# Optimization experiments

Hardware: AMD Instinct MI355X
Metric: run time of the kernel (lower is better)

The kernel has to match this reference:

```python
import jax, jax.numpy as jnp
import numpy as np

R, D, H, NLAYERS = 128, 64, 64, 3
B, N = 64, 1024
INIT_W = 0.1


def setup_inputs() -> dict:
    key = jax.random.key(0)
    ks = jax.random.split(key, 10)
    x = jax.random.normal(ks[0], (B, D, N), dtype=jnp.float32)
    L = jax.random.randint(ks[1], (B, 1, N), 0, 2, dtype=jnp.int32)
    wq0 = INIT_W * jax.random.normal(ks[2], (R, D), dtype=jnp.float32)
    wqr = INIT_W * jax.random.normal(ks[3], (NLAYERS - 1, R, R), dtype=jnp.float32)
    wk0 = INIT_W * jax.random.normal(ks[4], (R, D), dtype=jnp.float32)
    wkr = INIT_W * jax.random.normal(ks[5], (NLAYERS - 1, R, R), dtype=jnp.float32)
    wv0 = INIT_W * jax.random.normal(ks[6], (R, D), dtype=jnp.float32)
    wvr = INIT_W * jax.random.normal(ks[7], (NLAYERS - 1, R, R), dtype=jnp.float32)
    wor = INIT_W * jax.random.normal(ks[8], (NLAYERS - 1, R, R), dtype=jnp.float32)
    wo_last = INIT_W * jax.random.normal(ks[9], (H, R), dtype=jnp.float32)
    return {"x": x, "L": L, "wq0": wq0, "wqr": wqr, "wk0": wk0, "wkr": wkr,
            "wv0": wv0, "wvr": wvr, "wor": wor, "wo_last": wo_last}


def reference(x, L, wq0, wqr, wk0, wkr, wv0, wvr, wor, wo_last):
    # x: [B, d, N]; L: [B, 1, N] neighbor mask (first row used)
    Lrow = L[:, 0, :].astype(jnp.float32)                      # [B, N]
    num_neighbors = jnp.sum((Lrow >= 1).astype(jnp.float32), axis=1)[:, None, None] + 1.0  # [B,1,1]
    scale = jnp.sqrt(num_neighbors)
    mask = Lrow[:, None, :]                                    # [B, 1, N], broadcast over r

    inp = x
    for layer in range(NLAYERS):
        Wq = wq0 if layer == 0 else wqr[layer - 1]
        Wk = wk0 if layer == 0 else wkr[layer - 1]
        Wv = wv0 if layer == 0 else wvr[layer - 1]
        # sigmoid-gated projections: [B, r, N]
        Q = jax.nn.sigmoid(jnp.einsum('rd,bdn->brn', Wq, inp))
        K = jax.nn.sigmoid(jnp.einsum('rd,bdn->brn', Wk, inp))
        V = jax.nn.sigmoid(jnp.einsum('rd,bdn->brn', Wv, inp))
        # degree-scaled softmax attention over agents: scores [B, N, N]
        A = jax.nn.softmax(jnp.einsum('brn,brm->bnm', Q, K) / scale, axis=-1)
        # o[b,r,n] = sum_m A[b,n,m] * V[b,r,m]  -> [B, r, N]
        o = jnp.einsum('bnm,brm->brn', A, V)
        Wo = wor[layer] if layer < NLAYERS - 1 else wo_last
        inp = jax.nn.silu(jnp.einsum('or,brn->bon', Wo, o))
        if layer != NLAYERS - 1:  # remask_bias=True
            inp = mask * inp
    return inp  # [B, h, N]
```

## Files before the change

kernel.cpp:

```cpp
#include <hip/hip_runtime.h>


typedef __bf16 bf16;
typedef bf16 bf16x2 __attribute__((ext_vector_type(2)));
typedef bf16 bf16x4 __attribute__((ext_vector_type(4)));
typedef bf16 bf16x8 __attribute__((ext_vector_type(8)));
typedef float f32x4 __attribute__((ext_vector_type(4)));
typedef float f32x16 __attribute__((ext_vector_type(16)));

#define MFMA32(a, b, c) __builtin_amdgcn_mfma_f32_32x32x16_bf16(a, b, c, 0, 0, 0)
#define ZERO16 {0,0,0,0,0,0,0,0,0,0,0,0,0,0,0,0}
#define LOG2E 1.44269504f

__device__ __forceinline__ float fast_exp2(float x) {
  return __builtin_amdgcn_exp2f(x);
}
__device__ __forceinline__ float fast_sigmoid(float x) {
  return __builtin_amdgcn_rcpf(1.0f + fast_exp2(-LOG2E * x));
}

__global__ __launch_bounds__(256) void prep_kernel(
    const int* __restrict__ L,
    const float* __restrict__ wq0, const float* __restrict__ wqr,
    const float* __restrict__ wk0, const float* __restrict__ wkr,
    const float* __restrict__ wv0, const float* __restrict__ wvr,
    const float* __restrict__ wor, const float* __restrict__ wo_last,
    float* __restrict__ scale_inv, float* __restrict__ biasv,
    bf16* __restrict__ wbf) {
  __shared__ int red[256];
  const int blk = blockIdx.x;
  const int tid = threadIdx.x;
  if (blk < 64) {
    int cnt = 0;
    for (int n = tid; n < 1024; n += 256) cnt += (L[blk * 1024 + n] >= 1) ? 1 : 0;
    red[tid] = cnt;
    __syncthreads();
    for (int s = 128; s > 0; s >>= 1) {
      if (tid < s) red[tid] += red[tid + s];
      __syncthreads();
    }
    if (tid == 0) {
      float iv = rsqrtf((float)red[0] + 1.0f);
      scale_inv[blk] = iv;
      biasv[blk] = fmaxf(0.0f, 128.0f * iv * LOG2E - 80.0f);
    }
  } else {
    for (int i = (blk - 64) * 256 + tid; i < 163840; i += 64 * 256) {
      float v;
      if      (i <   8192) v = wq0[i];
      else if (i <  40960) v = wqr[i - 8192];
      else if (i <  49152) v = wk0[i - 40960];
      else if (i <  81920) v = wkr[i - 49152];
      else if (i <  90112) v = wv0[i - 81920];
      else if (i < 122880) v = wvr[i - 90112];
      else if (i < 155648) v = wor[i - 122880];
      else                 v = wo_last[i - 155648];
      wbf[i] = (bf16)v;
    }
  }
}

__global__ __launch_bounds__(256) void xk0_kernel(
    const float* __restrict__ x, const bf16* __restrict__ Wk,
    const bf16* __restrict__ Wv, bf16* __restrict__ xT,
    bf16* __restrict__ Kt, bf16* __restrict__ Vn) {
  __shared__ float tile[64][65];
  __shared__ __attribute__((aligned(16))) bf16 inp_lds[64 * 72];
  const int tid = threadIdx.x;
  const int lane = tid & 63, wv = tid >> 6;
  const int la = lane & 31, hi = lane >> 5;
  const int b = blockIdx.x >> 4;
  const int t0 = (blockIdx.x & 15) * 64;

  {
    const int nl = tid & 63, dbase = (tid >> 6) * 16;
#pragma unroll
    for (int i = 0; i < 16; i++) {
      int d = dbase + i;
      tile[d][nl] = x[(size_t)(b * 64 + d) * 1024 + t0 + nl];
    }
  }
  __syncthreads();
  {
    const int dl = (tid & 31) * 2, nb = (tid >> 5) * 8;
#pragma unroll
    for (int i = 0; i < 8; i++) {
      int n = nb + i;
      bf16x2 pr = {(bf16)tile[dl][n], (bf16)tile[dl + 1][n]};
      *(bf16x2*)(xT + (size_t)(b * 1024 + t0 + n) * 64 + dl) = pr;
      *(bf16x2*)&inp_lds[n * 72 + dl] = pr;
    }
  }
  __syncthreads();

  const int sub = wv & 1;
  if (wv < 2) {
#pragma unroll
    for (int rt2 = 0; rt2 < 2; rt2++) {
      const int rt = 2 * sub + rt2;
      bf16x8 wf[4];
#pragma unroll
      for (int ks = 0; ks < 4; ks++)
        wf[ks] = *(const bf16x8*)(Wk + (size_t)(la + 32 * rt) * 64 + hi * 8 + ks * 16);
#pragma unroll
      for (int tt = 0; tt < 2; tt++) {
        f32x16 acc = ZERO16;
#pragma unroll
        for (int ks = 0; ks < 4; ks++) {
          bf16x8 bfr = *(const bf16x8*)&inp_lds[(la + 32 * tt) * 72 + hi * 8 + ks * 16];
          acc = MFMA32(wf[ks], bfr, acc);
        }
#pragma unroll
        for (int g = 0; g < 4; g++) {
          bf16x4 pk;
#pragma unroll
          for (int i = 0; i < 4; i++) pk[i] = (bf16)fast_sigmoid(acc[4 * g + i]);
          *(bf16x4*)(Kt + (size_t)(b * 1024 + t0 + 32 * tt + la) * 128 +
                     32 * rt + 8 * g + 4 * hi) = pk;
        }
      }
    }
  } else {
#pragma unroll
    for (int rc2 = 0; rc2 < 2; rc2++) {
      const int rc = 2 * sub + rc2;
      bf16x8 wf[4];
#pragma unroll
      for (int ks = 0; ks < 4; ks++)
        wf[ks] = *(const bf16x8*)(Wv + (size_t)(la + 32 * rc) * 64 + hi * 8 + ks * 16);
#pragma unroll
      for (int tt = 0; tt < 2; tt++) {
        f32x16 acc = ZERO16;
#pragma unroll
        for (int ks = 0; ks < 4; ks++) {
          bf16x8 afr = *(const bf16x8*)&inp_lds[(la + 32 * tt) * 72 + hi * 8 + ks * 16];
          acc = MFMA32(afr, wf[ks], acc);
        }
#pragma unroll
        for (int g = 0; g < 4; g++) {
          bf16x4 pk;
#pragma unroll
          for (int i = 0; i < 4; i++) pk[i] = (bf16)fast_sigmoid(acc[4 * g + i]);
          *(bf16x4*)(Vn + (size_t)(b * 128 + la + 32 * rc) * 1024 +
                     t0 + 32 * tt + 8 * g + 4 * hi) = pk;
        }
      }
    }
  }
}

template <int DIN>
__global__ __launch_bounds__(256) void kv_kernel(
    const bf16* __restrict__ inpT, const bf16* __restrict__ Wk,
    const bf16* __restrict__ Wv, bf16* __restrict__ Kt,
    bf16* __restrict__ Vn) {
  constexpr int SIN = DIN + 8;
  constexpr int KS = DIN / 16;
  constexpr int CPR = DIN / 8;
  __shared__ __attribute__((aligned(16))) bf16 inp_lds[64 * SIN];
  const int tid = threadIdx.x;
  const int lane = tid & 63, wv = tid >> 6;
  const int la = lane & 31, hi = lane >> 5;
  const int b = blockIdx.x >> 4;
  const int t0 = (blockIdx.x & 15) * 64;

  for (int i = tid; i < 64 * CPR; i += 256) {
    int row = i / CPR, c = i % CPR;
    *(bf16x8*)&inp_lds[row * SIN + c * 8] =
        *(const bf16x8*)(inpT + (size_t)(b * 1024 + t0 + row) * DIN + c * 8);
  }
  __syncthreads();

  const int sub = wv & 1;
  if (wv < 2) {
#pragma unroll
    for (int rt2 = 0; rt2 < 2; rt2++) {
      const int rt = 2 * sub + rt2;
      bf16x8 wf[KS];
#pragma unroll
      for (int ks = 0; ks < KS; ks++)
        wf[ks] = *(const bf16x8*)(Wk + (size_t)(la + 32 * rt) * DIN + hi * 8 + ks * 16);
#pragma unroll
      for (int tt = 0; tt < 2; tt++) {
        f32x16 acc = ZERO16;
#pragma unroll
        for (int ks = 0; ks < KS; ks++) {
          bf16x8 bfr = *(const bf16x8*)&inp_lds[(la + 32 * tt) * SIN + hi * 8 + ks * 16];
          acc = MFMA32(wf[ks], bfr, acc);
        }
#pragma unroll
        for (int g = 0; g < 4; g++) {
          bf16x4 pk;
#pragma unroll
          for (int i = 0; i < 4; i++) pk[i] = (bf16)fast_sigmoid(acc[4 * g + i]);
          *(bf16x4*)(Kt + (size_t)(b * 1024 + t0 + 32 * tt + la) * 128 +
                     32 * rt + 8 * g + 4 * hi) = pk;
        }
      }
    }
  } else {
#pragma unroll
    for (int rc2 = 0; rc2 < 2; rc2++) {
      const int rc = 2 * sub + rc2;
      bf16x8 wf[KS];
#pragma unroll
      for (int ks = 0; ks < KS; ks++)
        wf[ks] = *(const bf16x8*)(Wv + (size_t)(la + 32 * rc) * DIN + hi * 8 + ks * 16);
#pragma unroll
      for (int tt = 0; tt < 2; tt++) {
        f32x16 acc = ZERO16;
#pragma unroll
        for (int ks = 0; ks < KS; ks++) {
          bf16x8 afr = *(const bf16x8*)&inp_lds[(la + 32 * tt) * SIN + hi * 8 + ks * 16];
          acc = MFMA32(afr, wf[ks], acc);
        }
#pragma unroll
        for (int g = 0; g < 4; g++) {
          bf16x4 pk;
#pragma unroll
          for (int i = 0; i < 4; i++) pk[i] = (bf16)fast_sigmoid(acc[4 * g + i]);
          *(bf16x4*)(Vn + (size_t)(b * 128 + la + 32 * rc) * 1024 +
                     t0 + 32 * tt + 8 * g + 4 * hi) = pk;
        }
      }
    }
  }
}

template <int DIN>
__global__ __launch_bounds__(256, 2) void flash_kernel(
    const bf16* __restrict__ inpT, const bf16* __restrict__ Wq,
    const bf16* __restrict__ Kt, const bf16* __restrict__ Vn,
    const float* __restrict__ scale_inv, const float* __restrict__ biasv,
    const int* __restrict__ L, const bf16* __restrict__ Wo,
    void* __restrict__ outp, int last,
    const bf16* __restrict__ Wkn, const bf16* __restrict__ Wvn,
    bf16* __restrict__ Ktn, bf16* __restrict__ Vnn, int kvgen) {
  __shared__ __attribute__((aligned(16))) char smem[70656];
  bf16* K_lds = (bf16*)smem;
  bf16* V_lds = (bf16*)(smem + 17408);
  bf16* P_lds = (bf16*)(smem + 35840);

  const int tid = threadIdx.x;
  const int lane = tid & 63, wv = tid >> 6;
  const int la = lane & 31, hi = lane >> 5;
  const int xcd = blockIdx.x & 7;
  const int kk = blockIdx.x >> 3;
  const int b = xcd * 8 + (kk & 7);
  const int q0 = (kk >> 3) * 128;

  const float inv2 = scale_inv[b] * LOG2E;
  const float bb = biasv[b];

  {
    constexpr int SIN = DIN + 8;
    constexpr int KSD = DIN / 16;
    constexpr int CPR = DIN / 8;
    bf16* inp_s = (bf16*)smem;
    for (int i = tid; i < 128 * CPR; i += 256) {
      int row = i / CPR, c = i % CPR;
      *(bf16x8*)&inp_s[row * SIN + c * 8] =
          *(const bf16x8*)(inpT + (size_t)(b * 1024 + q0 + row) * DIN + c * 8);
    }
    __syncthreads();
    bf16* Q_lds = (bf16*)(smem + 35840);
    bf16x8 wf[KSD];
#pragma unroll
    for (int ks = 0; ks < KSD; ks++)
      wf[ks] = *(const bf16x8*)(Wq + (size_t)(la + 32 * wv) * DIN + hi * 8 + ks * 16);
#pragma unroll
    for (int nt = 0; nt < 4; nt++) {
      f32x16 acc = ZERO16;
#pragma unroll
      for (int ks = 0; ks < KSD; ks++) {
        bf16x8 bfr = *(const bf16x8*)&inp_s[(la + 32 * nt) * SIN + hi * 8 + ks * 16];
        acc = MFMA32(wf[ks], bfr, acc);
      }
#pragma unroll
      for (int g = 0; g < 4; g++) {
        bf16x4 pk;
#pragma unroll
        for (int i = 0; i < 4; i++)
          pk[i] = (bf16)(fast_sigmoid(acc[4 * g + i]) * inv2);
        *(bf16x4*)&Q_lds[(size_t)(32 * nt + la) * 136 + 32 * wv + 8 * g + 4 * hi] = pk;
      }
    }
    __syncthreads();
  }

  const int ms = wv & 1, nw = wv >> 1;
  bf16x8 qB[2][8];
#pragma unroll
  for (int nt = 0; nt < 2; nt++)
#pragma unroll
    for (int ks = 0; ks < 8; ks++)
      qB[nt][ks] = *(const bf16x8*)((bf16*)(smem + 35840) +
                                    (size_t)(64 * nw + 32 * nt + la) * 136 +
                                    hi * 8 + ks * 16);

  const int krow = tid >> 4, kc = (tid & 15) * 8;
  const int vrow = tid >> 3, vc = (tid & 7) * 8;
  const bf16* kbase = Kt + (size_t)b * 1024 * 128;
  const bf16* vbase = Vn + (size_t)b * 128 * 1024;
  bf16x8 kr[4], vr[4];
#pragma unroll
  for (int p = 0; p < 4; p++) {
    kr[p] = *(const bf16x8*)(kbase + (size_t)(krow + 16 * p) * 128 + kc);
    vr[p] = *(const bf16x8*)(vbase + (size_t)(vrow + 32 * p) * 1024 + vc);
  }

  const int nh = wv & 1, rh = wv >> 1;
  f32x16 acc_o[2][2] = {{ZERO16, ZERO16}, {ZERO16, ZERO16}};
  float rs[2] = {0.f, 0.f};

  for (int it = 0; it < 16; it++) {
    __syncthreads();
#pragma unroll
    for (int p = 0; p < 4; p++)
      *(bf16x8*)&K_lds[(krow + 16 * p) * 136 + kc] = kr[p];
#pragma unroll
    for (int p = 0; p < 4; p++)
      *(bf16x8*)&V_lds[(vrow + 32 * p) * 72 + vc] = vr[p];
    __syncthreads();

    if (it < 15) {
      const int m1 = (it + 1) * 64;
#pragma unroll
      for (int p = 0; p < 4; p++) {
        kr[p] = *(const bf16x8*)(kbase + (size_t)(m1 + krow + 16 * p) * 128 + kc);
        vr[p] = *(const bf16x8*)(vbase + (size_t)(vrow + 32 * p) * 1024 + m1 + vc);
      }
    }

    bf16x8 kf[8];
#pragma unroll
    for (int ks = 0; ks < 8; ks++)
      kf[ks] = *(const bf16x8*)&K_lds[(32 * ms + la) * 136 + hi * 8 + ks * 16];
#pragma unroll
    for (int nt = 0; nt < 2; nt++) {
      f32x16 sa = ZERO16;
#pragma unroll
      for (int ks = 0; ks < 8; ks++) sa = MFMA32(kf[ks], qB[nt][ks], sa);
#pragma unroll
      for (int g = 0; g < 4; g++) {
        bf16x4 pk;
#pragma unroll
        for (int i = 0; i < 4; i++) {
          float p = fast_exp2(sa[4 * g + i] - bb);
          rs[nt] += p;
          pk[i] = (bf16)p;
        }
        *(bf16x4*)&P_lds[(size_t)(64 * nw + 32 * nt + la) * 72 +
                         32 * ms + 8 * g + 4 * hi] = pk;
      }
    }
    __syncthreads();

    bf16x8 pA[2][4];
#pragma unroll
    for (int nt2 = 0; nt2 < 2; nt2++)
#pragma unroll
      for (int k2 = 0; k2 < 4; k2++)
        pA[nt2][k2] = *(const bf16x8*)&P_lds[(size_t)(64 * nh + 32 * nt2 + la) * 72 +
                                             hi * 8 + k2 * 16];
#pragma unroll
    for (int rt = 0; rt < 2; rt++) {
#pragma unroll
      for (int k2 = 0; k2 < 4; k2++) {
        bf16x8 vB = *(const bf16x8*)&V_lds[(size_t)(64 * rh + 32 * rt + la) * 72 +
                                           hi * 8 + k2 * 16];
        acc_o[0][rt] = MFMA32(pA[0][k2], vB, acc_o[0][rt]);
        acc_o[1][rt] = MFMA32(pA[1][k2], vB, acc_o[1][rt]);
      }
    }
  }

  rs[0] += __shfl_xor(rs[0], 32, 64);
  rs[1] += __shfl_xor(rs[1], 32, 64);
  __syncthreads();
  float* rsp = (float*)smem;
  if (lane < 32) {
    rsp[ms * 128 + 64 * nw + la] = rs[0];
    rsp[ms * 128 + 64 * nw + 32 + la] = rs[1];
  }
  __syncthreads();

  bf16* O_lds = (bf16*)(smem + 35840);
#pragma unroll
  for (int nt2 = 0; nt2 < 2; nt2++) {
#pragma unroll
    for (int g = 0; g < 4; g++) {
      const int nb = 64 * nh + 32 * nt2 + 8 * g + 4 * hi;
      f32x4 ra = *(f32x4*)&rsp[nb];
      f32x4 rc = *(f32x4*)&rsp[128 + nb];
      f32x4 is;
#pragma unroll
      for (int i = 0; i < 4; i++) is[i] = 1.0f / (ra[i] + rc[i]);
#pragma unroll
      for (int rt = 0; rt < 2; rt++) {
#pragma unroll
        for (int i = 0; i < 4; i++) {
          O_lds[(size_t)(nb + i) * 136 + 64 * rh + 32 * rt + la] =
              (bf16)(acc_o[nt2][rt][4 * g + i] * is[i]);
        }
      }
    }
  }
  __syncthreads();

  if (!last) {
    bf16* out_b = (bf16*)outp;
    bf16* O2 = (bf16*)smem;
    const int* Lg = L + b * 1024 + q0;
    bf16x8 wB[8];
#pragma unroll
    for (int ks = 0; ks < 8; ks++)
      wB[ks] = *(const bf16x8*)(Wo + (size_t)(la + 32 * wv) * 128 + hi * 8 + ks * 16);
#pragma unroll
    for (int nt = 0; nt < 4; nt++) {
      f32x16 acc = ZERO16;
#pragma unroll
      for (int ks = 0; ks < 8; ks++) {
        bf16x8 oA = *(const bf16x8*)&O_lds[(size_t)(la + 32 * nt) * 136 +
                                           hi * 8 + ks * 16];
        acc = MFMA32(oA, wB[ks], acc);
      }
#pragma unroll
      for (int g = 0; g < 4; g++) {
#pragma unroll
        for (int i = 0; i < 4; i++) {
          int n = 32 * nt + 8 * g + 4 * hi + i;
          float xv = acc[4 * g + i];
          float y = xv * fast_sigmoid(xv) * (float)Lg[n];
          out_b[(size_t)(b * 1024 + q0 + n) * 128 + 32 * wv + la] = (bf16)y;
          if (kvgen) O2[(size_t)n * 136 + 32 * wv + la] = (bf16)y;
        }
      }
    }
    if (kvgen) {
      __syncthreads();
      const bf16* O2c = (const bf16*)smem;
      const int sub = wv & 1;
      const bf16* W2 = (wv < 2) ? Wkn : Wvn;
#pragma unroll
      for (int rt2 = 0; rt2 < 2; rt2++) {
        const int rt = 2 * sub + rt2;
        bf16x8 wf[8];
#pragma unroll
        for (int ks = 0; ks < 8; ks++)
          wf[ks] = *(const bf16x8*)(W2 + (size_t)(la + 32 * rt) * 128 +
                                    hi * 8 + ks * 16);
#pragma unroll
        for (int tt = 0; tt < 4; tt++) {
          f32x16 acc = ZERO16;
          if (wv < 2) {
#pragma unroll
            for (int ks = 0; ks < 8; ks++) {
              bf16x8 bB = *(const bf16x8*)&O2c[(size_t)(32 * tt + la) * 136 +
                                               hi * 8 + ks * 16];
              acc = MFMA32(wf[ks], bB, acc);
            }
#pragma unroll
            for (int g = 0; g < 4; g++) {
              bf16x4 pk;
#pragma unroll
              for (int i = 0; i < 4; i++) pk[i] = (bf16)fast_sigmoid(acc[4 * g + i]);
              *(bf16x4*)(Ktn + (size_t)(b * 1024 + q0 + 32 * tt + la) * 128 +
                         32 * rt + 8 * g + 4 * hi) = pk;
            }
          } else {
#pragma unroll
            for (int ks = 0; ks < 8; ks++) {
              bf16x8 aA = *(const bf16x8*)&O2c[(size_t)(32 * tt + la) * 136 +
                                               hi * 8 + ks * 16];
              acc = MFMA32(aA, wf[ks], acc);
            }
#pragma unroll
            for (int g = 0; g < 4; g++) {
              bf16x4 pk;
#pragma unroll
              for (int i = 0; i < 4; i++) pk[i] = (bf16)fast_sigmoid(acc[4 * g + i]);
              *(bf16x4*)(Vnn + (size_t)(b * 128 + 32 * rt + la) * 1024 +
                         q0 + 32 * tt + 8 * g + 4 * hi) = pk;
            }
          }
        }
      }
    }
  } else {
    const int hs = wv & 1, nq = wv >> 1;
    float* outf = (float*)outp;
    bf16x8 wA[8];
#pragma unroll
    for (int ks = 0; ks < 8; ks++)
      wA[ks] = *(const bf16x8*)(Wo + (size_t)(la + 32 * hs) * 128 + hi * 8 + ks * 16);
#pragma unroll
    for (int t = 0; t < 2; t++) {
      const int ns4 = nq + 2 * t;
      f32x16 acc = ZERO16;
#pragma unroll
      for (int ks = 0; ks < 8; ks++) {
        bf16x8 oB = *(const bf16x8*)&O_lds[(size_t)(32 * ns4 + la) * 136 +
                                           hi * 8 + ks * 16];
        acc = MFMA32(wA[ks], oB, acc);
      }
#pragma unroll
      for (int g = 0; g < 4; g++) {
#pragma unroll
        for (int i = 0; i < 4; i++) {
          int h = 32 * hs + 8 * g + 4 * hi + i;
          float xv = acc[4 * g + i];
          outf[(size_t)(b * 64 + h) * 1024 + q0 + 32 * ns4 + la] =
              xv * fast_sigmoid(xv);
        }
      }
    }
  }
}

__global__ __launch_bounds__(256) void xpose_kernel(const float* __restrict__ x,
                                                    bf16* __restrict__ xT) {
  __shared__ float tile[64][65];
  const int blk = blockIdx.x;
  const int b = blk >> 4;
  const int n0 = (blk & 15) * 64;
  const int tid = threadIdx.x;
  {
    const int nl = tid & 63, dbase = (tid >> 6) * 16;
#pragma unroll
    for (int i = 0; i < 16; i++) {
      int d = dbase + i;
      tile[d][nl] = x[(size_t)(b * 64 + d) * 1024 + n0 + nl];
    }
  }
  __syncthreads();
  {
    const int dl = (tid & 31) * 2, nb = (tid >> 5) * 8;
#pragma unroll
    for (int i = 0; i < 8; i++) {
      int n = nb + i;
      bf16x2 pr = {(bf16)tile[dl][n], (bf16)tile[dl + 1][n]};
      *(bf16x2*)(xT + (size_t)(b * 1024 + n0 + n) * 64 + dl) = pr;
    }
  }
}

extern "C" void kernel_launch(void* const* d_in, const int* in_sizes, int n_in,
                              void* d_out, int out_size, void* d_ws, size_t ws_size,
                              hipStream_t stream) {
  const float* x = (const float*)d_in[0];
  const int* L = (const int*)d_in[1];
  const float* wq0 = (const float*)d_in[2];
  const float* wqr = (const float*)d_in[3];
  const float* wk0 = (const float*)d_in[4];
  const float* wkr = (const float*)d_in[5];
  const float* wv0 = (const float*)d_in[6];
  const float* wvr = (const float*)d_in[7];
  const float* wor = (const float*)d_in[8];
  const float* wo_last = (const float*)d_in[9];

  char* ws = (char*)d_ws;
  float* scale_inv = (float*)(ws + 0);
  float* biasv = (float*)(ws + 1024);
  bf16* wbf = (bf16*)(ws + 4096);
  bf16* xT = (bf16*)(ws + 335872);
  bf16* inpT = (bf16*)(ws + 8724480);
  bf16* KtA = (bf16*)(ws + 25501696);
  bf16* VnA = (bf16*)(ws + 42278912);
  bf16* KtB = (bf16*)(ws + 59056128);
  bf16* VnB = (bf16*)(ws + 75833344);

  prep_kernel<<<128, 256, 0, stream>>>(L, wq0, wqr, wk0, wkr, wv0, wvr, wor,
                                       wo_last, scale_inv, biasv, wbf);

  if (ws_size >= 92610560) {
    xk0_kernel<<<1024, 256, 0, stream>>>(x, wbf + 40960, wbf + 81920, xT, KtA, VnA);
    flash_kernel<64><<<512, 256, 0, stream>>>(
        xT, wbf + 0, KtA, VnA, scale_inv, biasv, L, wbf + 122880, (void*)inpT, 0,
        wbf + 49152, wbf + 90112, KtB, VnB, 1);
    flash_kernel<128><<<512, 256, 0, stream>>>(
        inpT, wbf + 8192, KtB, VnB, scale_inv, biasv, L, wbf + 139264,
        (void*)inpT, 0, wbf + 65536, wbf + 106496, KtA, VnA, 1);
    flash_kernel<128><<<512, 256, 0, stream>>>(
        inpT, wbf + 24576, KtA, VnA, scale_inv, biasv, L, wbf + 155648, d_out, 1,
        nullptr, nullptr, nullptr, nullptr, 0);
  } else if (ws_size >= 59056128) {
    xpose_kernel<<<1024, 256, 0, stream>>>(x, xT);
    for (int l = 0; l < 3; l++) {
      const bf16* Wq = (l == 0) ? wbf + 0 : wbf + 8192 + (size_t)(l - 1) * 16384;
      const bf16* Wk = (l == 0) ? wbf + 40960 : wbf + 49152 + (size_t)(l - 1) * 16384;
      const bf16* Wv = (l == 0) ? wbf + 81920 : wbf + 90112 + (size_t)(l - 1) * 16384;
      const bf16* Wo = (l < 2) ? wbf + 122880 + (size_t)l * 16384 : wbf + 155648;
      void* outp = (l < 2) ? (void*)inpT : (void*)d_out;
      if (l == 0) {
        kv_kernel<64><<<1024, 256, 0, stream>>>(xT, Wk, Wv, KtA, VnA);
        flash_kernel<64><<<512, 256, 0, stream>>>(xT, Wq, KtA, VnA, scale_inv,
                                                  biasv, L, Wo, outp, 0,
                                                  nullptr, nullptr, nullptr,
                                                  nullptr, 0);
      } else {
        kv_kernel<128><<<1024, 256, 0, stream>>>(inpT, Wk, Wv, KtA, VnA);
        flash_kernel<128><<<512, 256, 0, stream>>>(inpT, Wq, KtA, VnA, scale_inv,
                                                   biasv, L, Wo, outp,
                                                   (l == 2) ? 1 : 0, nullptr,
                                                   nullptr, nullptr, nullptr, 0);
      }
    }
  }
}
```

Before: 268.6 us.

## Keep P and Q in registers via permlane swaps and double-buffer K/V tiles

The flash kernel is restructured so each wave owns 32 query rows end to end. Q fragments and softmax probabilities P are converted to bf16 MFMA operand layout in registers using cvt_pk_bf16 and permlane32_swap, which removes the Q/P round trips through LDS. K/V tiles are double-buffered in LDS with a two-tile-ahead register prefetch, cutting the barriers per iteration from three to one. The cross-wave row-sum exchange also becomes a per-wave reduction. The cost is higher register pressure from four f32x16 accumulators plus the Q fragments, under a 2-blocks-per-SM launch bound, and slightly more LDS.

```diff
diff --git a/kernel.cpp b/kernel.cpp
--- a/kernel.cpp
+++ b/kernel.cpp
@@ -7,6 +7,8 @@
 typedef bf16 bf16x8 __attribute__((ext_vector_type(8)));
 typedef float f32x4 __attribute__((ext_vector_type(4)));
 typedef float f32x16 __attribute__((ext_vector_type(16)));
+typedef unsigned int u32;
+typedef u32 u32x4 __attribute__((ext_vector_type(4)));
 
 #define MFMA32(a, b, c) __builtin_amdgcn_mfma_f32_32x32x16_bf16(a, b, c, 0, 0, 0)
 #define ZERO16 {0,0,0,0,0,0,0,0,0,0,0,0,0,0,0,0}
@@ -17,6 +19,32 @@
 }
 __device__ __forceinline__ float fast_sigmoid(float x) {
   return __builtin_amdgcn_rcpf(1.0f + fast_exp2(-LOG2E * x));
+}
+__device__ __forceinline__ u32 cvt_pk_bf16(float lo, float hi) {
+  u32 r;
+  asm("v_cvt_pk_bf16_f32 %0, %1, %2" : "=v"(r) : "v"(lo), "v"(hi));
+  return r;
+}
+__device__ __forceinline__ void pl32_swap(u32& a, u32& b) {
+  asm("v_permlane32_swap_b32 %0, %1" : "+v"(a), "+v"(b));
+}
+__device__ __forceinline__ void build_frags(const f32x16 v, bf16x8& f0, bf16x8& f1) {
+  u32 t0 = cvt_pk_bf16(v[0], v[1]);
+  u32 t1 = cvt_pk_bf16(v[2], v[3]);
+  u32 t2 = cvt_pk_bf16(v[4], v[5]);
+  u32 t3 = cvt_pk_bf16(v[6], v[7]);
+  pl32_swap(t0, t2);
+  pl32_swap(t1, t3);
+  u32x4 a = {t0, t1, t2, t3};
+  f0 = __builtin_bit_cast(bf16x8, a);
+  u32 s0 = cvt_pk_bf16(v[8], v[9]);
+  u32 s1 = cvt_pk_bf16(v[10], v[11]);
+  u32 s2 = cvt_pk_bf16(v[12], v[13]);
+  u32 s3 = cvt_pk_bf16(v[14], v[15]);
+  pl32_swap(s0, s2);
+  pl32_swap(s1, s3);
+  u32x4 c = {s0, s1, s2, s3};
+  f1 = __builtin_bit_cast(bf16x8, c);
 }
 
 __global__ __launch_bounds__(256) void prep_kernel(
@@ -219,7 +247,7 @@
           bf16x4 pk;
 #pragma unroll
           for (int i = 0; i < 4; i++) pk[i] = (bf16)fast_sigmoid(acc[4 * g + i]);
-          *(bf16x4*)(Vn + (size_t)(b * 128 + la + 32 * rc) * 1024 +
+          *(bf16x4*)(Vn + (size_t)(b * 128 + 32 * rc + la) * 1024 +
                      t0 + 32 * tt + 8 * g + 4 * hi) = pk;
         }
       }
@@ -236,10 +264,7 @@
     void* __restrict__ outp, int last,
     const bf16* __restrict__ Wkn, const bf16* __restrict__ Wvn,
     bf16* __restrict__ Ktn, bf16* __restrict__ Vnn, int kvgen) {
-  __shared__ __attribute__((aligned(16))) char smem[70656];
-  bf16* K_lds = (bf16*)smem;
-  bf16* V_lds = (bf16*)(smem + 17408);
-  bf16* P_lds = (bf16*)(smem + 35840);
+  __shared__ __attribute__((aligned(16))) char smem[71680];
 
   const int tid = threadIdx.x;
   const int lane = tid & 63, wv = tid >> 6;
@@ -252,6 +277,19 @@
   const float inv2 = scale_inv[b] * LOG2E;
   const float bb = biasv[b];
 
+  const int krow = tid >> 4, kc = (tid & 15) * 8;
+  const int vrow = tid >> 3, vc = (tid & 7) * 8;
+  const bf16* kbase = Kt + (size_t)b * 1024 * 128;
+  const bf16* vbase = Vn + (size_t)b * 128 * 1024;
+
+  bf16x8 kr[4], vr[4];
+#pragma unroll
+  for (int p = 0; p < 4; p++) {
+    kr[p] = *(const bf16x8*)(kbase + (size_t)(krow + 16 * p) * 128 + kc);
+    vr[p] = *(const bf16x8*)(vbase + (size_t)(vrow + 32 * p) * 1024 + vc);
+  }
+
+  bf16x8 qB[8];
   {
     constexpr int SIN = DIN + 8;
     constexpr int KSD = DIN / 16;
@@ -263,146 +301,115 @@
           *(const bf16x8*)(inpT + (size_t)(b * 1024 + q0 + row) * DIN + c * 8);
     }
     __syncthreads();
-    bf16* Q_lds = (bf16*)(smem + 35840);
-    bf16x8 wf[KSD];
+    bf16x8 bfr[KSD];
 #pragma unroll
     for (int ks = 0; ks < KSD; ks++)
-      wf[ks] = *(const bf16x8*)(Wq + (size_t)(la + 32 * wv) * DIN + hi * 8 + ks * 16);
-#pragma unroll
-    for (int nt = 0; nt < 4; nt++) {
+      bfr[ks] = *(const bf16x8*)&inp_s[(32 * wv + la) * SIN + hi * 8 + ks * 16];
+#pragma unroll
+    for (int rt = 0; rt < 4; rt++) {
       f32x16 acc = ZERO16;
 #pragma unroll
       for (int ks = 0; ks < KSD; ks++) {
-        bf16x8 bfr = *(const bf16x8*)&inp_s[(la + 32 * nt) * SIN + hi * 8 + ks * 16];
-        acc = MFMA32(wf[ks], bfr, acc);
-      }
-#pragma unroll
-      for (int g = 0; g < 4; g++) {
-        bf16x4 pk;
-#pragma unroll
-        for (int i = 0; i < 4; i++)
-          pk[i] = (bf16)(fast_sigmoid(acc[4 * g + i]) * inv2);
-        *(bf16x4*)&Q_lds[(size_t)(32 * nt + la) * 136 + 32 * wv + 8 * g + 4 * hi] = pk;
-      }
+        bf16x8 wf = *(const bf16x8*)(Wq + (size_t)(32 * rt + la) * DIN +
+                                     hi * 8 + ks * 16);
+        acc = MFMA32(wf, bfr[ks], acc);
+      }
+      f32x16 qv;
+#pragma unroll
+      for (int j = 0; j < 16; j++) qv[j] = fast_sigmoid(acc[j]) * inv2;
+      build_frags(qv, qB[2 * rt], qB[2 * rt + 1]);
     }
     __syncthreads();
   }
 
-  const int ms = wv & 1, nw = wv >> 1;
-  bf16x8 qB[2][8];
-#pragma unroll
-  for (int nt = 0; nt < 2; nt++)
-#pragma unroll
-    for (int ks = 0; ks < 8; ks++)
-      qB[nt][ks] = *(const bf16x8*)((bf16*)(smem + 35840) +
-                                    (size_t)(64 * nw + 32 * nt + la) * 136 +
-                                    hi * 8 + ks * 16);
-
-  const int krow = tid >> 4, kc = (tid & 15) * 8;
-  const int vrow = tid >> 3, vc = (tid & 7) * 8;
-  const bf16* kbase = Kt + (size_t)b * 1024 * 128;
-  const bf16* vbase = Vn + (size_t)b * 128 * 1024;
-  bf16x8 kr[4], vr[4];
-#pragma unroll
-  for (int p = 0; p < 4; p++) {
-    kr[p] = *(const bf16x8*)(kbase + (size_t)(krow + 16 * p) * 128 + kc);
-    vr[p] = *(const bf16x8*)(vbase + (size_t)(vrow + 32 * p) * 1024 + vc);
-  }
-
-  const int nh = wv & 1, rh = wv >> 1;
-  f32x16 acc_o[2][2] = {{ZERO16, ZERO16}, {ZERO16, ZERO16}};
-  float rs[2] = {0.f, 0.f};
+  {
+    bf16* K0 = (bf16*)smem;
+    bf16* V0 = (bf16*)(smem + 34816);
+#pragma unroll
+    for (int p = 0; p < 4; p++) *(bf16x8*)&K0[(krow + 16 * p) * 136 + kc] = kr[p];
+#pragma unroll
+    for (int p = 0; p < 4; p++) *(bf16x8*)&V0[(vrow + 32 * p) * 72 + vc] = vr[p];
+#pragma unroll
+    for (int p = 0; p < 4; p++) {
+      kr[p] = *(const bf16x8*)(kbase + (size_t)(64 + krow + 16 * p) * 128 + kc);
+      vr[p] = *(const bf16x8*)(vbase + (size_t)(vrow + 32 * p) * 1024 + 64 + vc);
+    }
+    __syncthreads();
+  }
+
+  f32x16 acc_o[4] = {ZERO16, ZERO16, ZERO16, ZERO16};
+  float rs = 0.f;
 
   for (int it = 0; it < 16; it++) {
+    const int cur = it & 1;
+    const bf16* Kc = (const bf16*)(smem + cur * 17408);
+    const bf16* Vc = (const bf16*)(smem + 34816 + cur * 18432);
+    if (it < 15) {
+      bf16* Kn = (bf16*)(smem + (1 - cur) * 17408);
+      bf16* Vx = (bf16*)(smem + 34816 + (1 - cur) * 18432);
+#pragma unroll
+      for (int p = 0; p < 4; p++)
+        *(bf16x8*)&Kn[(krow + 16 * p) * 136 + kc] = kr[p];
+#pragma unroll
+      for (int p = 0; p < 4; p++)
+        *(bf16x8*)&Vx[(vrow + 32 * p) * 72 + vc] = vr[p];
+    }
+    if (it < 14) {
+      const int m2 = (it + 2) * 64;
+#pragma unroll
+      for (int p = 0; p < 4; p++) {
+        kr[p] = *(const bf16x8*)(kbase + (size_t)(m2 + krow + 16 * p) * 128 + kc);
+        vr[p] = *(const bf16x8*)(vbase + (size_t)(vrow + 32 * p) * 1024 + m2 + vc);
+      }
+    }
+
+    bf16x8 pa[4];
+#pragma unroll
+    for (int kt = 0; kt < 2; kt++) {
+      f32x16 sa = ZERO16;
+#pragma unroll
+      for (int ks = 0; ks < 8; ks++) {
+        bf16x8 kf = *(const bf16x8*)&Kc[(32 * kt + la) * 136 + hi * 8 + ks * 16];
+        sa = MFMA32(kf, qB[ks], sa);
+      }
+      f32x16 pv;
+#pragma unroll
+      for (int j = 0; j < 16; j++) {
+        float p = fast_exp2(sa[j] - bb);
+        rs += p;
+        pv[j] = p;
+      }
+      build_frags(pv, pa[2 * kt], pa[2 * kt + 1]);
+    }
+
+#pragma unroll
+    for (int rt = 0; rt < 4; rt++) {
+#pragma unroll
+      for (int k2 = 0; k2 < 4; k2++) {
+        bf16x8 vB = *(const bf16x8*)&Vc[(32 * rt + la) * 72 + hi * 8 + k2 * 16];
+        acc_o[rt] = MFMA32(pa[k2], vB, acc_o[rt]);
+      }
+    }
     __syncthreads();
-#pragma unroll
-    for (int p = 0; p < 4; p++)
-      *(bf16x8*)&K_lds[(krow + 16 * p) * 136 + kc] = kr[p];
-#pragma unroll
-    for (int p = 0; p < 4; p++)
-      *(bf16x8*)&V_lds[(vrow + 32 * p) * 72 + vc] = vr[p];
-    __syncthreads();
-
-    if (it < 15) {
-      const int m1 = (it + 1) * 64;
-#pragma unroll
-      for (int p = 0; p < 4; p++) {
-        kr[p] = *(const bf16x8*)(kbase + (size_t)(m1 + krow + 16 * p) * 128 + kc);
-        vr[p] = *(const bf16x8*)(vbase + (size_t)(vrow + 32 * p) * 1024 + m1 + vc);
-      }
-    }
-
-    bf16x8 kf[8];
-#pragma unroll
-    for (int ks = 0; ks < 8; ks++)
-      kf[ks] = *(const bf16x8*)&K_lds[(32 * ms + la) * 136 + hi * 8 + ks * 16];
-#pragma unroll
-    for (int nt = 0; nt < 2; nt++) {
-      f32x16 sa = ZERO16;
-#pragma unroll
-      for (int ks = 0; ks < 8; ks++) sa = MFMA32(kf[ks], qB[nt][ks], sa);
-#pragma unroll
-      for (int g = 0; g < 4; g++) {
-        bf16x4 pk;
-#pragma unroll
-        for (int i = 0; i < 4; i++) {
-          float p = fast_exp2(sa[4 * g + i] - bb);
-          rs[nt] += p;
-          pk[i] = (bf16)p;
-        }
-        *(bf16x4*)&P_lds[(size_t)(64 * nw + 32 * nt + la) * 72 +
-                         32 * ms + 8 * g + 4 * hi] = pk;
-      }
-    }
-    __syncthreads();
-
-    bf16x8 pA[2][4];
-#pragma unroll
-    for (int nt2 = 0; nt2 < 2; nt2++)
-#pragma unroll
-      for (int k2 = 0; k2 < 4; k2++)
-        pA[nt2][k2] = *(const bf16x8*)&P_lds[(size_t)(64 * nh + 32 * nt2 + la) * 72 +
-                                             hi * 8 + k2 * 16];
-#pragma unroll
-    for (int rt = 0; rt < 2; rt++) {
-#pragma unroll
-      for (int k2 = 0; k2 < 4; k2++) {
-        bf16x8 vB = *(const bf16x8*)&V_lds[(size_t)(64 * rh + 32 * rt + la) * 72 +
-                                           hi * 8 + k2 * 16];
-        acc_o[0][rt] = MFMA32(pA[0][k2], vB, acc_o[0][rt]);
-        acc_o[1][rt] = MFMA32(pA[1][k2], vB, acc_o[1][rt]);
-      }
-    }
-  }
-
-  rs[0] += __shfl_xor(rs[0], 32, 64);
-  rs[1] += __shfl_xor(rs[1], 32, 64);
-  __syncthreads();
-  float* rsp = (float*)smem;
-  if (lane < 32) {
-    rsp[ms * 128 + 64 * nw + la] = rs[0];
-    rsp[ms * 128 + 64 * nw + 32 + la] = rs[1];
-  }
-  __syncthreads();
-
-  bf16* O_lds = (bf16*)(smem + 35840);
-#pragma unroll
-  for (int nt2 = 0; nt2 < 2; nt2++) {
-#pragma unroll
-    for (int g = 0; g < 4; g++) {
-      const int nb = 64 * nh + 32 * nt2 + 8 * g + 4 * hi;
-      f32x4 ra = *(f32x4*)&rsp[nb];
-      f32x4 rc = *(f32x4*)&rsp[128 + nb];
-      f32x4 is;
-#pragma unroll
-      for (int i = 0; i < 4; i++) is[i] = 1.0f / (ra[i] + rc[i]);
-#pragma unroll
-      for (int rt = 0; rt < 2; rt++) {
-#pragma unroll
-        for (int i = 0; i < 4; i++) {
-          O_lds[(size_t)(nb + i) * 136 + 64 * rh + 32 * rt + la] =
-              (bf16)(acc_o[nt2][rt][4 * g + i] * is[i]);
-        }
+  }
+
+  rs += __shfl_xor(rs, 32, 64);
+  float* rsp = (float*)(smem + 34816);
+  if (lane < 32) rsp[32 * wv + la] = rs;
+  bf16* O_lds = (bf16*)smem;
+#pragma unroll
+  for (int g = 0; g < 4; g++) {
+    const int qb = 8 * g + 4 * hi;
+    f32x4 r4 = *(f32x4*)&rsp[32 * wv + qb];
+    f32x4 is;
+#pragma unroll
+    for (int i = 0; i < 4; i++) is[i] = 1.0f / r4[i];
+#pragma unroll
+    for (int rt = 0; rt < 4; rt++) {
+#pragma unroll
+      for (int i = 0; i < 4; i++) {
+        O_lds[(size_t)(32 * wv + qb + i) * 136 + 32 * rt + la] =
+            (bf16)(acc_o[rt][4 * g + i] * is[i]);
       }
     }
   }
@@ -410,7 +417,7 @@
 
   if (!last) {
     bf16* out_b = (bf16*)outp;
-    bf16* O2 = (bf16*)smem;
+    bf16* O2 = (bf16*)(smem + 36864);
     const int* Lg = L + b * 1024 + q0;
     bf16x8 wB[8];
 #pragma unroll
@@ -439,7 +446,7 @@
     }
     if (kvgen) {
       __syncthreads();
-      const bf16* O2c = (const bf16*)smem;
+      const bf16* O2c = (const bf16*)(smem + 36864);
       const int sub = wv & 1;
       const bf16* W2 = (wv < 2) ? Wkn : Wvn;
 #pragma unroll
```

Result: no change. 273.6 us (+1.9%).
